# Kernel optimization log

Measured on AMD Instinct MI355X. Metric: run time of the kernel, lower is better.

The kernel has to match this reference:

```python
import jax, jax.numpy as jnp
import numpy as np

BS, L, S, AMB = 64, 64, 63, 32   # batch, sentence len, opseq steps, ambiguities per step
H, E, V, MLP = 128, 300, 50000, 1024
EPS = 1e-8


def setup_inputs() -> dict:
    key = jax.random.key(0)
    ks = jax.random.split(key, 12)
    u = lambda k, shp: jax.random.uniform(k, shp, dtype=jnp.float32) * 0.1
    return {
        "sentences1": jax.random.randint(ks[0], (BS, L), 0, V, dtype=jnp.int32),
        "operations1": jax.random.randint(ks[1], (BS, S, 2 * AMB), 0, L, dtype=jnp.int32),
        "oopl1": jnp.full((BS,), L + S, dtype=jnp.int32),
        "sentences2": jax.random.randint(ks[2], (BS, L), 0, V, dtype=jnp.int32),
        "operations2": jax.random.randint(ks[3], (BS, S, 2 * AMB), 0, L, dtype=jnp.int32),
        "oopl2": jnp.full((BS,), L + S, dtype=jnp.int32),
        "W": u(ks[4], (5 * H, E)),
        "U": u(ks[5], (5 * H, 2 * H)),
        "b": jnp.zeros((5 * H,), dtype=jnp.float32),
        "energy_u": u(ks[6], (H,)),
        "unk_embedding": u(ks[7], (E,)),
        "word_embeddings": jax.random.normal(ks[8], (V, E), dtype=jnp.float32),
        "A": u(ks[9], (MLP, 4 * H)),
        "a": u(ks[10], (MLP,)),
        "inv_temperature": jnp.float32(1.0),
    }


def _gates(preact, ccL, ccR):
    # preact: [..., 5H]; tree-LSTM cell (i, fL, fR, o, u gates)
    i = jax.nn.sigmoid(preact[..., :H])
    fL = jax.nn.sigmoid(preact[..., H:2 * H])
    fR = jax.nn.sigmoid(preact[..., 2 * H:3 * H])
    o = jax.nn.sigmoid(preact[..., 3 * H:4 * H])
    u = jnp.tanh(preact[..., 4 * H:5 * H])
    c = fL * ccL + fR * ccR + i * u
    h = o * jnp.tanh(c)
    return c, h


def _run_chart(sentences, operations, W, U, b, energy_u, unk_embedding,
               word_embeddings, inv_temperature):
    bs = sentences.shape[0]
    # leaf phase: embed each word, preact = W @ emb + b, ccL = ccR = 0
    emb = jnp.where(sentences[..., None] >= 0,
                    word_embeddings[jnp.clip(sentences, 0)], unk_embedding)  # [bs,L,E]
    preact = jnp.einsum('ble,ge->blg', emb, W) + b                            # [bs,L,5H]
    c, h = _gates(preact, 0.0, 0.0)
    chart = jnp.zeros((bs, L + S, 2 * H), dtype=jnp.float32)
    chart = chart.at[:, :L, :].set(jnp.concatenate([c, h], axis=-1))

    def step(chart, inp):
        ops, pos = inp                                   # ops: [bs, 2*AMB], pos: scalar
        entries = jnp.take_along_axis(chart, ops[:, :, None].astype(jnp.int32), axis=1)
        entries = entries.reshape(bs, AMB, 2, 2 * H)     # [bs, amb, (L,R), 2H]
        ccL = entries[:, :, 0, :H]
        ccR = entries[:, :, 1, :H]
        hh = entries[:, :, :, H:].reshape(bs, AMB, 2 * H)  # concat(hL, hR)
        pre = jnp.einsum('bak,gk->bag', hh, U) + b         # [bs, amb, 5H]
        c, h = _gates(pre, ccL, ccR)
        # cosine similarity of h against energy_u
        hn = jnp.maximum(jnp.sqrt(jnp.sum(h * h, axis=-1)), EPS)
        un = jnp.maximum(jnp.sqrt(jnp.sum(energy_u * energy_u)), EPS)
        e = jnp.einsum('bah,h->ba', h, energy_u) / (hn * un)
        s = jax.nn.softmax(e * inv_temperature, axis=1)    # [bs, amb]
        combined = jnp.concatenate([jnp.einsum('ba,bah->bh', s, c),
                                    jnp.einsum('ba,bah->bh', s, h)], axis=-1)
        chart = jax.lax.dynamic_update_slice(chart, combined[:, None, :], (0, pos, 0))
        return chart, None

    ops_seq = jnp.swapaxes(operations, 0, 1)             # [S, bs, 2*AMB]
    positions = L + jnp.arange(S, dtype=jnp.int32)
    chart, _ = jax.lax.scan(step, chart, (ops_seq, positions))
    return chart


def reference(sentences1, operations1, oopl1, sentences2, operations2, oopl2,
              W, U, b, energy_u, unk_embedding, word_embeddings, A, a,
              inv_temperature):
    chart1 = _run_chart(sentences1, operations1, W, U, b, energy_u,
                        unk_embedding, word_embeddings, inv_temperature)
    chart2 = _run_chart(sentences2, operations2, W, U, b, energy_u,
                        unk_embedding, word_embeddings, inv_temperature)
    bs = chart1.shape[0]
    bidx = jnp.arange(bs)
    s1 = chart1[bidx, oopl1 - 1, H:]                     # final composed h, [bs, H]
    s2 = chart2[bidx, oopl2 - 1, H:]
    u = (s1 - s2) ** 2
    v = s1 * s2
    conc = jnp.concatenate([u, v, s1, s2], axis=1)       # [bs, 4H]
    out = jax.nn.relu(jnp.einsum('jk,ik->ij', A, conc) + a)
    return out
```

## Files before the change

kernel.cpp:

```cpp
#include <hip/hip_runtime.h>
#include <hip/hip_bf16.h>

#define BSZ 64
#define LL  64
#define SS  63
#define AMB 32
#define HH  128
#define EE  300
#define MLPN 1024
#define GG  640
#define K2  256
#define PP  127
#define CROW 272

typedef __attribute__((ext_vector_type(8))) short short8;
typedef __attribute__((ext_vector_type(4))) float f32x4;

__device__ __forceinline__ float sigf(float x) { return 1.f / (1.f + __expf(-x)); }

__device__ __forceinline__ unsigned short f2bf(float x) {
    unsigned int u = __float_as_uint(x);
    u += 0x7fffu + ((u >> 16) & 1u);
    return (unsigned short)(u >> 16);
}
__device__ __forceinline__ float bf2f(short x) {
    return __uint_as_float(((unsigned)(unsigned short)x) << 16);
}

#define PW 25600
#define PU 20480
__global__ void __launch_bounds__(256) prep_kernel(
        const float* __restrict__ W, const float* __restrict__ U,
        short* __restrict__ WTB, short* __restrict__ UTB) {
    int idx = blockIdx.x * 256 + threadIdx.x;
    if (idx < PW) {
        int lane = idx & 63, r = idx >> 6;
        int kk = r % 10, n = r / 10;
        int g = n * 16 + (lane & 15);
        int k0 = kk * 32 + ((lane >> 4) << 3);
        const float* src = W + (size_t)g * EE + k0;
        float f[8];
        if (k0 + 8 <= EE) {
            f32x4 x0 = *(const f32x4*)src;
            f32x4 x1 = *(const f32x4*)(src + 4);
            f[0]=x0[0]; f[1]=x0[1]; f[2]=x0[2]; f[3]=x0[3];
            f[4]=x1[0]; f[5]=x1[1]; f[6]=x1[2]; f[7]=x1[3];
        } else {
#pragma unroll
            for (int j = 0; j < 8; ++j) f[j] = (k0 + j < EE) ? src[j] : 0.f;
        }
        short8 v;
#pragma unroll
        for (int j = 0; j < 8; ++j) v[j] = (short)f2bf(f[j]);
        *(short8*)(WTB + (size_t)idx * 8) = v;
    } else if (idx < PW + PU) {
        int o = idx - PW;
        int lane = o & 63, r = o >> 6;
        int kk = r & 7, n = r >> 3;
        int g = n * 16 + (lane & 15);
        int k0 = kk * 32 + ((lane >> 4) << 3);
        const float* src = U + (size_t)g * K2 + k0;
        f32x4 x0 = *(const f32x4*)src;
        f32x4 x1 = *(const f32x4*)(src + 4);
        short8 v;
        v[0]=(short)f2bf(x0[0]); v[1]=(short)f2bf(x0[1]); v[2]=(short)f2bf(x0[2]); v[3]=(short)f2bf(x0[3]);
        v[4]=(short)f2bf(x1[0]); v[5]=(short)f2bf(x1[1]); v[6]=(short)f2bf(x1[2]); v[7]=(short)f2bf(x1[3]);
        *(short8*)(UTB + (size_t)o * 8) = v;
    }
}

__global__ void __launch_bounds__(1024) main_kernel(
        const int* __restrict__ sent1, const int* __restrict__ sent2,
        const int* __restrict__ ops1, const int* __restrict__ ops2,
        const int* __restrict__ oopl1, const int* __restrict__ oopl2,
        const short* __restrict__ WTB, const short* __restrict__ UTB,
        const float* __restrict__ bias, const float* __restrict__ eu,
        const float* __restrict__ invt,
        const float* __restrict__ unk, const float* __restrict__ wemb,
        float* __restrict__ fin) {
    __shared__ __align__(16) short chartL[127 * CROW + 16];
    __shared__ __align__(16) char  buf[40960];
    __shared__ int ops_all[SS * 64];
    __shared__ int sent_lds[64];
    __shared__ unsigned long long smask[64];
    __shared__ int live_list[SS];
    __shared__ float e_num[AMB], h2s[AMB], s_w[AMB];
    __shared__ float comb[2][2][HH];
    __shared__ int nl_sh;
    __shared__ float un_sh;

    short8* AsL = (short8*)buf;
    short8* As2 = (short8*)buf;
    float*  chh = (float*)(buf + 16384);

    const int tid = threadIdx.x;
    const int pair = blockIdx.x, ch = pair >> 6, b = pair & 63;
    const int* sent = ch ? sent2 : sent1;
    const int* ops  = ch ? ops2 : ops1;
    const int* oopl = ch ? oopl2 : oopl1;
    const float it = invt[0];
    const int w = tid >> 6, lane = tid & 63, quad = lane >> 4, l15 = lane & 15;

#pragma unroll
    for (int i = 0; i < 4; ++i) {
        int idx = i * 1024 + tid;
        if (idx < SS * 64) ops_all[idx] = min(max(ops[b * SS * 64 + idx], 0), PP - 1);
    }
    if (tid < 64) sent_lds[tid] = sent[b * LL + tid];
    if (tid < 64) {
        float v = eu[tid] * eu[tid] + eu[tid + 64] * eu[tid + 64];
        for (int off = 32; off >= 1; off >>= 1) v += __shfl_xor(v, off);
        if (tid == 0) un_sh = fmaxf(sqrtf(v), 1e-8f);
    }
    __syncthreads();

#pragma unroll
    for (int i = 0; i < 4; ++i) {
        int t = i * 16 + w;
        if (t < SS) {
            int q = ops_all[t * 64 + lane] - LL;
            unsigned long long bit = (q >= 0 && q < t) ? (1ull << q) : 0ull;
            for (int off = 32; off >= 1; off >>= 1) bit |= __shfl_xor(bit, off);
            if (lane == 0) smask[t] = bit;
        }
    }
    __syncthreads();

    if (tid == 0) {
        unsigned long long mask = 0ull;
        int q0 = oopl[b] - 1 - LL;
        if (q0 >= 0) { if (q0 > SS - 1) q0 = SS - 1; mask = 1ull << q0; }
        for (int t = SS - 1; t >= 1; --t)
            if ((mask >> t) & 1) mask |= smask[t];
        int n = 0;
        for (int t = 0; t < SS; ++t)
            if ((mask >> t) & 1) live_list[n++] = t;
        nl_sh = n;
    }

#pragma unroll
    for (int i = 0; i < 3; ++i) {
        int idx = i * 1024 + tid;
        if (idx < 2142)
            ((int4*)(chartL + 64 * CROW))[idx] = make_int4(0, 0, 0, 0);
    }
    {
        float ef[3][8];
        int est[3], eso[3];
#pragma unroll
        for (int i = 0; i < 3; ++i) {
            int slot = i * 1024 + tid;
            est[i] = -1;
            if (slot < 2560) {
                int t = slot / 40, oct = slot - t * 40;
                est[i] = t; eso[i] = oct;
                int s = sent_lds[t];
                const float* src = (s >= 0) ? (wemb + (size_t)s * EE) : unk;
                int k0 = oct * 8;
                if (k0 + 8 <= EE) {
                    f32x4 x0 = *(const f32x4*)(src + k0);
                    f32x4 x1 = *(const f32x4*)(src + k0 + 4);
                    ef[i][0]=x0[0]; ef[i][1]=x0[1]; ef[i][2]=x0[2]; ef[i][3]=x0[3];
                    ef[i][4]=x1[0]; ef[i][5]=x1[1]; ef[i][6]=x1[2]; ef[i][7]=x1[3];
                } else {
#pragma unroll
                    for (int j = 0; j < 8; ++j) ef[i][j] = (k0 + j < EE) ? src[k0 + j] : 0.f;
                }
            }
        }
#pragma unroll
        for (int i = 0; i < 3; ++i) {
            if (est[i] >= 0) {
                int t = est[i], oct = eso[i];
                short8 v;
#pragma unroll
                for (int j = 0; j < 8; ++j) v[j] = (short)f2bf(ef[i][j]);
                AsL[((t >> 4) * 10 + (oct >> 2)) * 64 + ((oct & 3) << 4) + (t & 15)] = v;
            }
        }
    }
    __syncthreads();

    {
        const int mt = w & 3, nug = w >> 2;
        f32x4 acc[2][3] = {};
        for (int kk = 0; kk < 10; ++kk) {
            short8 a0 = AsL[(mt * 10 + kk) * 64 + lane];
#pragma unroll
            for (int si = 0; si < 3; ++si) {
                int s5 = (si == 0) ? 0 : (si == 1 ? 3 : 4);
#pragma unroll
                for (int hf = 0; hf < 2; ++hf) {
                    int n = (nug + hf * 4) + 8 * s5;
                    short8 bv = *(const short8*)(WTB + ((size_t)(n * 10 + kk) * 64 + lane) * 8);
                    acc[hf][si] = __builtin_amdgcn_mfma_f32_16x16x32_bf16(a0, bv, acc[hf][si], 0, 0, 0);
                }
            }
        }
#pragma unroll
        for (int hf = 0; hf < 2; ++hf) {
            int jc = (nug + hf * 4) * 16 + l15;
            float bi = bias[jc], bo = bias[3 * HH + jc], bu = bias[4 * HH + jc];
#pragma unroll
            for (int r = 0; r < 4; ++r) {
                float pi = acc[hf][0][r] + bi;
                float po = acc[hf][1][r] + bo;
                float pu = acc[hf][2][r] + bu;
                float cv = sigf(pi) * tanhf(pu);
                float hv = sigf(po) * tanhf(cv);
                int l = mt * 16 + quad * 4 + r;
                chartL[l * CROW + jc]      = (short)f2bf(cv);
                chartL[l * CROW + HH + jc] = (short)f2bf(hv);
            }
        }
    }
    __syncthreads();

    const int nl = nl_sh;
    const float eul = eu[lane], euh = eu[64 + lane];
    const int smt = w & 1, snu = w >> 1;
    const int sjc = snu * 16 + l15;
    const float bi  = bias[sjc],          bfl = bias[HH + sjc];
    const float bfr = bias[2 * HH + sjc], bo  = bias[3 * HH + sjc];
    const float bu  = bias[4 * HH + sjc];

    for (int sidx = 0; sidx < nl; ++sidx) {
        const int t = live_list[sidx];
        const int* oprow = ops_all + t * 64;

        {
            int a = tid >> 5, oct = tid & 31, side = oct >> 4, m8 = oct & 15;
            int row = oprow[2 * a + side];
            short8 v = *(const short8*)(chartL + row * CROW + HH + m8 * 8);
            As2[((a >> 4) * 8 + (oct >> 2)) * 64 + ((oct & 3) << 4) + (a & 15)] = v;
        }
        __syncthreads();

        float cvals[4], hvals[4];
        {
            f32x4 acc[5] = {};
            for (int kk = 0; kk < 8; ++kk) {
                short8 a0 = As2[(smt * 8 + kk) * 64 + lane];
#pragma unroll
                for (int s5 = 0; s5 < 5; ++s5) {
                    short8 bv = *(const short8*)(UTB + ((size_t)((snu + 8 * s5) * 8 + kk) * 64 + lane) * 8);
                    acc[s5] = __builtin_amdgcn_mfma_f32_16x16x32_bf16(a0, bv, acc[s5], 0, 0, 0);
                }
            }
#pragma unroll
            for (int r = 0; r < 4; ++r) {
                int a = smt * 16 + quad * 4 + r;
                float ccLv = bf2f(chartL[oprow[2 * a] * CROW + sjc]);
                float ccRv = bf2f(chartL[oprow[2 * a + 1] * CROW + sjc]);
                float cv = sigf(acc[1][r] + bfl) * ccLv
                         + sigf(acc[2][r] + bfr) * ccRv
                         + sigf(acc[0][r] + bi) * tanhf(acc[4][r] + bu);
                float hv = sigf(acc[3][r] + bo) * tanhf(cv);
                cvals[r] = cv; hvals[r] = hv;
                chh[a * 132 + sjc] = hv;
            }
        }
        __syncthreads();

#pragma unroll
        for (int i = 0; i < 2; ++i) {
            int a = w * 2 + i;
            float h0 = chh[a * 132 + lane], h1 = chh[a * 132 + 64 + lane];
            float pe = h0 * eul + h1 * euh;
            float pn = h0 * h0 + h1 * h1;
            for (int off = 32; off >= 1; off >>= 1) {
                pe += __shfl_xor(pe, off);
                pn += __shfl_xor(pn, off);
            }
            if (lane == 0) { e_num[a] = pe; h2s[a] = pn; }
        }
        __syncthreads();

        if (tid < 64) {
            float v = (tid < AMB)
                ? (e_num[tid] / (fmaxf(sqrtf(h2s[tid]), 1e-8f) * un_sh)) * it
                : -3.4e38f;
            float m = v;
            for (int off = 32; off >= 1; off >>= 1) m = fmaxf(m, __shfl_xor(m, off));
            float ex = (tid < AMB) ? __expf(v - m) : 0.f;
            float su = ex;
            for (int off = 32; off >= 1; off >>= 1) su += __shfl_xor(su, off);
            if (tid < AMB) s_w[tid] = ex / su;
        }
        __syncthreads();

        {
            float sc = 0.f, sh = 0.f;
#pragma unroll
            for (int r = 0; r < 4; ++r) {
                int a = smt * 16 + quad * 4 + r;
                float sw = s_w[a];
                sc = fmaf(sw, cvals[r], sc);
                sh = fmaf(sw, hvals[r], sh);
            }
            sc += __shfl_xor(sc, 16); sc += __shfl_xor(sc, 32);
            sh += __shfl_xor(sh, 16); sh += __shfl_xor(sh, 32);
            if (lane < 16) {
                comb[smt][0][sjc] = sc;
                comb[smt][1][sjc] = sh;
            }
        }
        __syncthreads();
        if (tid < K2) {
            int part = tid >> 7, col = tid & 127;
            float val = comb[0][part][col] + comb[1][part][col];
            chartL[(LL + t) * CROW + part * HH + col] = (short)f2bf(val);
        }
        __syncthreads();
    }

    int p = min(max(oopl[b] - 1, 0), PP - 1);
    if (tid < K2)
        fin[(size_t)pair * K2 + tid] = bf2f(chartL[p * CROW + tid]);
}

__global__ void __launch_bounds__(256) mlp_kernel(
        const float* __restrict__ fin,
        const float* __restrict__ A, const float* __restrict__ abias,
        float* __restrict__ out) {
    __shared__ __align__(16) float conc[4][512];
    const int tid = threadIdx.x;
    const int jt = blockIdx.x & 15, bt = blockIdx.x >> 4;

#pragma unroll
    for (int i = 0; i < 2; ++i) {
        int s = i * 256 + tid;
        int bl = s >> 7, kv = s & 127;
        int k0 = kv * 4, sel = k0 >> 7, kk0 = k0 & 127;
        int b = bt * 4 + bl;
        f32x4 s1 = *(const f32x4*)(fin + (size_t)b * K2 + HH + kk0);
        f32x4 s2 = *(const f32x4*)(fin + (size_t)(BSZ + b) * K2 + HH + kk0);
        f32x4 v;
        if (sel == 0)      { f32x4 d = s1 - s2; v = d * d; }
        else if (sel == 1) v = s1 * s2;
        else if (sel == 2) v = s1;
        else               v = s2;
        *(f32x4*)&conc[bl][k0] = v;
    }
    __syncthreads();

    const int jj = tid & 63, bg = tid >> 6;
    const int j = jt * 64 + jj, b = bt * 4 + bg;
    const float* Arow = A + (size_t)j * 512;
    float acc0 = abias[j], acc1 = 0.f;
    for (int k = 0; k < 512; k += 8) {
        f32x4 a0 = *(const f32x4*)(Arow + k);
        f32x4 a1 = *(const f32x4*)(Arow + k + 4);
        f32x4 c0 = *(const f32x4*)&conc[bg][k];
        f32x4 c1 = *(const f32x4*)&conc[bg][k + 4];
#pragma unroll
        for (int u = 0; u < 4; ++u) {
            acc0 = fmaf(a0[u], c0[u], acc0);
            acc1 = fmaf(a1[u], c1[u], acc1);
        }
    }
    out[(size_t)b * MLPN + j] = fmaxf(acc0 + acc1, 0.f);
}

extern "C" void kernel_launch(void* const* d_in, const int* in_sizes, int n_in,
                              void* d_out, int out_size, void* d_ws, size_t ws_size,
                              hipStream_t stream) {
    const int*   sent1 = (const int*)d_in[0];
    const int*   ops1  = (const int*)d_in[1];
    const int*   oopl1 = (const int*)d_in[2];
    const int*   sent2 = (const int*)d_in[3];
    const int*   ops2  = (const int*)d_in[4];
    const int*   oopl2 = (const int*)d_in[5];
    const float* W     = (const float*)d_in[6];
    const float* U     = (const float*)d_in[7];
    const float* bias  = (const float*)d_in[8];
    const float* eu    = (const float*)d_in[9];
    const float* unk   = (const float*)d_in[10];
    const float* wemb  = (const float*)d_in[11];
    const float* A     = (const float*)d_in[12];
    const float* ab    = (const float*)d_in[13];
    const float* invt  = (const float*)d_in[14];
    float* out = (float*)d_out;
    (void)in_sizes; (void)n_in; (void)out_size; (void)ws_size;

    char* ws = (char*)d_ws;
    const size_t WTB_OFF = 0;
    const size_t UTB_OFF = 409600;
    const size_t FIN_OFF = 737280;
    short* WTB = (short*)(ws + WTB_OFF);
    short* UTB = (short*)(ws + UTB_OFF);
    float* fin = (float*)(ws + FIN_OFF);

    prep_kernel<<<180, 256, 0, stream>>>(W, U, WTB, UTB);

    main_kernel<<<128, 1024, 0, stream>>>(sent1, sent2, ops1, ops2, oopl1, oopl2,
                                          WTB, UTB, bias, eu, invt, unk, wemb, fin);

    mlp_kernel<<<256, 256, 0, stream>>>(fin, A, ab, out);
}
```

Before: 186.9 us.

## Split leaf embedding GEMM into separate kernel across 256 blocks

The leaf phase (embedding gather, W projection via MFMA, gate activation) moves out of the per-sentence main kernel into its own kernel. That kernel uses 256 blocks, each handling half of a sentence, and writes bf16 c/h rows to a global chart buffer. The step kernel then loads the chart and ops with vectorized int4 reads. The leaf GEMM loop also double-buffers its W fragment loads. The aim is more parallelism for the leaf phase, since the old kernel used only 128 blocks. The cost is an extra kernel launch and a global round trip for the chart.

```diff
diff --git a/kernel.cpp b/kernel.cpp
--- a/kernel.cpp
+++ b/kernel.cpp
@@ -69,19 +69,104 @@
     }
 }
 
-__global__ void __launch_bounds__(1024) main_kernel(
+__global__ void __launch_bounds__(1024) leaf_kernel(
         const int* __restrict__ sent1, const int* __restrict__ sent2,
+        const short* __restrict__ WTB, const float* __restrict__ bias,
+        const float* __restrict__ unk, const float* __restrict__ wemb,
+        short* __restrict__ chartG) {
+    __shared__ __align__(16) short AsL[2 * 10 * 64 * 8];
+    const int tid = threadIdx.x;
+    const int blk = blockIdx.x, pair = blk >> 1, half = blk & 1;
+    const int ch = pair >> 6, b = pair & 63;
+    const int* sent = ch ? sent2 : sent1;
+    const int w = tid >> 6, lane = tid & 63, quad = lane >> 4, l15 = lane & 15;
+
+    {
+        float ef[2][8];
+        int est[2], eso[2];
+#pragma unroll
+        for (int i = 0; i < 2; ++i) {
+            int slot = i * 1024 + tid;
+            est[i] = -1;
+            if (slot < 1280) {
+                int tloc = slot / 40, oct = slot - tloc * 40;
+                est[i] = tloc; eso[i] = oct;
+                int sid = sent[b * LL + half * 32 + tloc];
+                const float* src = (sid >= 0) ? (wemb + (size_t)sid * EE) : unk;
+                int k0 = oct * 8;
+                if (k0 + 8 <= EE) {
+                    f32x4 x0 = *(const f32x4*)(src + k0);
+                    f32x4 x1 = *(const f32x4*)(src + k0 + 4);
+                    ef[i][0]=x0[0]; ef[i][1]=x0[1]; ef[i][2]=x0[2]; ef[i][3]=x0[3];
+                    ef[i][4]=x1[0]; ef[i][5]=x1[1]; ef[i][6]=x1[2]; ef[i][7]=x1[3];
+                } else {
+#pragma unroll
+                    for (int j = 0; j < 8; ++j) ef[i][j] = (k0 + j < EE) ? src[k0 + j] : 0.f;
+                }
+            }
+        }
+#pragma unroll
+        for (int i = 0; i < 2; ++i) {
+            if (est[i] >= 0) {
+                int tloc = est[i], oct = eso[i];
+                short8 v;
+#pragma unroll
+                for (int j = 0; j < 8; ++j) v[j] = (short)f2bf(ef[i][j]);
+                *(short8*)(AsL + (((tloc >> 4) * 10 + (oct >> 2)) * 64
+                                  + ((oct & 3) << 4) + (tloc & 15)) * 8) = v;
+            }
+        }
+    }
+    __syncthreads();
+
+    const int mt2 = w & 1, nu = w >> 1;
+    f32x4 acc[3] = {};
+    short8 bb0[3], bb1[3];
+#define LDW(dst, kkv) do { \
+    dst[0] = *(const short8*)(WTB + ((size_t)((nu +  0) * 10 + (kkv)) * 64 + lane) * 8); \
+    dst[1] = *(const short8*)(WTB + ((size_t)((nu + 24) * 10 + (kkv)) * 64 + lane) * 8); \
+    dst[2] = *(const short8*)(WTB + ((size_t)((nu + 32) * 10 + (kkv)) * 64 + lane) * 8); \
+} while (0)
+    LDW(bb0, 0);
+#pragma unroll 1
+    for (int kk = 0; kk < 10; kk += 2) {
+        LDW(bb1, kk + 1);
+        short8 a0 = *(const short8*)(AsL + ((mt2 * 10 + kk) * 64 + lane) * 8);
+        acc[0] = __builtin_amdgcn_mfma_f32_16x16x32_bf16(a0, bb0[0], acc[0], 0, 0, 0);
+        acc[1] = __builtin_amdgcn_mfma_f32_16x16x32_bf16(a0, bb0[1], acc[1], 0, 0, 0);
+        acc[2] = __builtin_amdgcn_mfma_f32_16x16x32_bf16(a0, bb0[2], acc[2], 0, 0, 0);
+        if (kk + 2 < 10) LDW(bb0, kk + 2);
+        short8 a1 = *(const short8*)(AsL + ((mt2 * 10 + kk + 1) * 64 + lane) * 8);
+        acc[0] = __builtin_amdgcn_mfma_f32_16x16x32_bf16(a1, bb1[0], acc[0], 0, 0, 0);
+        acc[1] = __builtin_amdgcn_mfma_f32_16x16x32_bf16(a1, bb1[1], acc[1], 0, 0, 0);
+        acc[2] = __builtin_amdgcn_mfma_f32_16x16x32_bf16(a1, bb1[2], acc[2], 0, 0, 0);
+    }
+#undef LDW
+
+    {
+        int jc = nu * 16 + l15;
+        float bi = bias[jc], bo = bias[3 * HH + jc], bu = bias[4 * HH + jc];
+        size_t pb = (size_t)pair * 16384;
+#pragma unroll
+        for (int r = 0; r < 4; ++r) {
+            float cv = sigf(acc[0][r] + bi) * tanhf(acc[2][r] + bu);
+            float hv = sigf(acc[1][r] + bo) * tanhf(cv);
+            int l = half * 32 + mt2 * 16 + quad * 4 + r;
+            chartG[pb + (size_t)l * 256 + jc]      = (short)f2bf(cv);
+            chartG[pb + (size_t)l * 256 + HH + jc] = (short)f2bf(hv);
+        }
+    }
+}
+
+__global__ void __launch_bounds__(1024) step_kernel(
         const int* __restrict__ ops1, const int* __restrict__ ops2,
         const int* __restrict__ oopl1, const int* __restrict__ oopl2,
-        const short* __restrict__ WTB, const short* __restrict__ UTB,
-        const float* __restrict__ bias, const float* __restrict__ eu,
-        const float* __restrict__ invt,
-        const float* __restrict__ unk, const float* __restrict__ wemb,
-        float* __restrict__ fin) {
+        const short* __restrict__ UTB, const float* __restrict__ bias,
+        const float* __restrict__ eu, const float* __restrict__ invt,
+        const short* __restrict__ chartG, float* __restrict__ fin) {
     __shared__ __align__(16) short chartL[127 * CROW + 16];
-    __shared__ __align__(16) char  buf[40960];
-    __shared__ int ops_all[SS * 64];
-    __shared__ int sent_lds[64];
+    __shared__ __align__(16) char  buf[33280];
+    __shared__ __align__(16) int ops_all[SS * 64];
     __shared__ unsigned long long smask[64];
     __shared__ int live_list[SS];
     __shared__ float e_num[AMB], h2s[AMB], s_w[AMB];
@@ -89,28 +174,45 @@
     __shared__ int nl_sh;
     __shared__ float un_sh;
 
-    short8* AsL = (short8*)buf;
     short8* As2 = (short8*)buf;
     float*  chh = (float*)(buf + 16384);
 
     const int tid = threadIdx.x;
     const int pair = blockIdx.x, ch = pair >> 6, b = pair & 63;
-    const int* sent = ch ? sent2 : sent1;
     const int* ops  = ch ? ops2 : ops1;
     const int* oopl = ch ? oopl2 : oopl1;
     const float it = invt[0];
     const int w = tid >> 6, lane = tid & 63, quad = lane >> 4, l15 = lane & 15;
 
-#pragma unroll
-    for (int i = 0; i < 4; ++i) {
-        int idx = i * 1024 + tid;
-        if (idx < SS * 64) ops_all[idx] = min(max(ops[b * SS * 64 + idx], 0), PP - 1);
-    }
-    if (tid < 64) sent_lds[tid] = sent[b * LL + tid];
+    const int4* cg = (const int4*)(chartG + (size_t)pair * 16384);
+    int4 c0 = cg[tid];
+    int4 c1 = cg[1024 + tid];
+    int4 opv = make_int4(0, 0, 0, 0);
+    if (tid < 1008) opv = ((const int4*)(ops + (size_t)b * SS * 64))[tid];
     if (tid < 64) {
         float v = eu[tid] * eu[tid] + eu[tid + 64] * eu[tid + 64];
         for (int off = 32; off >= 1; off >>= 1) v += __shfl_xor(v, off);
         if (tid == 0) un_sh = fmaxf(sqrtf(v), 1e-8f);
+    }
+#pragma unroll
+    for (int i = 0; i < 3; ++i) {
+        int idx = i * 1024 + tid;
+        if (idx < 2142)
+            ((int4*)(chartL + 64 * CROW))[idx] = make_int4(0, 0, 0, 0);
+    }
+    {
+        int r0 = tid >> 5, cq0 = tid & 31;
+        *(int4*)(chartL + r0 * CROW + (cq0 << 3)) = c0;
+        int t2 = 1024 + tid;
+        int r1 = t2 >> 5, cq1 = t2 & 31;
+        *(int4*)(chartL + r1 * CROW + (cq1 << 3)) = c1;
+    }
+    if (tid < 1008) {
+        opv.x = min(max(opv.x, 0), PP - 1);
+        opv.y = min(max(opv.y, 0), PP - 1);
+        opv.z = min(max(opv.z, 0), PP - 1);
+        opv.w = min(max(opv.w, 0), PP - 1);
+        ((int4*)ops_all)[tid] = opv;
     }
     __syncthreads();
 
@@ -136,83 +238,6 @@
         for (int t = 0; t < SS; ++t)
             if ((mask >> t) & 1) live_list[n++] = t;
         nl_sh = n;
-    }
-
-#pragma unroll
-    for (int i = 0; i < 3; ++i) {
-        int idx = i * 1024 + tid;
-        if (idx < 2142)
-            ((int4*)(chartL + 64 * CROW))[idx] = make_int4(0, 0, 0, 0);
-    }
-    {
-        float ef[3][8];
-        int est[3], eso[3];
-#pragma unroll
-        for (int i = 0; i < 3; ++i) {
-            int slot = i * 1024 + tid;
-            est[i] = -1;
-            if (slot < 2560) {
-                int t = slot / 40, oct = slot - t * 40;
-                est[i] = t; eso[i] = oct;
-                int s = sent_lds[t];
-                const float* src = (s >= 0) ? (wemb + (size_t)s * EE) : unk;
-                int k0 = oct * 8;
-                if (k0 + 8 <= EE) {
-                    f32x4 x0 = *(const f32x4*)(src + k0);
-                    f32x4 x1 = *(const f32x4*)(src + k0 + 4);
-                    ef[i][0]=x0[0]; ef[i][1]=x0[1]; ef[i][2]=x0[2]; ef[i][3]=x0[3];
-                    ef[i][4]=x1[0]; ef[i][5]=x1[1]; ef[i][6]=x1[2]; ef[i][7]=x1[3];
-                } else {
-#pragma unroll
-                    for (int j = 0; j < 8; ++j) ef[i][j] = (k0 + j < EE) ? src[k0 + j] : 0.f;
-                }
-            }
-        }
-#pragma unroll
-        for (int i = 0; i < 3; ++i) {
-            if (est[i] >= 0) {
-                int t = est[i], oct = eso[i];
-                short8 v;
-#pragma unroll
-                for (int j = 0; j < 8; ++j) v[j] = (short)f2bf(ef[i][j]);
-                AsL[((t >> 4) * 10 + (oct >> 2)) * 64 + ((oct & 3) << 4) + (t & 15)] = v;
-            }
-        }
-    }
-    __syncthreads();
-
-    {
-        const int mt = w & 3, nug = w >> 2;
-        f32x4 acc[2][3] = {};
-        for (int kk = 0; kk < 10; ++kk) {
-            short8 a0 = AsL[(mt * 10 + kk) * 64 + lane];
-#pragma unroll
-            for (int si = 0; si < 3; ++si) {
-                int s5 = (si == 0) ? 0 : (si == 1 ? 3 : 4);
-#pragma unroll
-                for (int hf = 0; hf < 2; ++hf) {
-                    int n = (nug + hf * 4) + 8 * s5;
-                    short8 bv = *(const short8*)(WTB + ((size_t)(n * 10 + kk) * 64 + lane) * 8);
-                    acc[hf][si] = __builtin_amdgcn_mfma_f32_16x16x32_bf16(a0, bv, acc[hf][si], 0, 0, 0);
-                }
-            }
-        }
-#pragma unroll
-        for (int hf = 0; hf < 2; ++hf) {
-            int jc = (nug + hf * 4) * 16 + l15;
-            float bi = bias[jc], bo = bias[3 * HH + jc], bu = bias[4 * HH + jc];
-#pragma unroll
-            for (int r = 0; r < 4; ++r) {
-                float pi = acc[hf][0][r] + bi;
-                float po = acc[hf][1][r] + bo;
-                float pu = acc[hf][2][r] + bu;
-                float cv = sigf(pi) * tanhf(pu);
-                float hv = sigf(po) * tanhf(cv);
-                int l = mt * 16 + quad * 4 + r;
-                chartL[l * CROW + jc]      = (short)f2bf(cv);
-                chartL[l * CROW + HH + jc] = (short)f2bf(hv);
-            }
-        }
     }
     __syncthreads();
 
@@ -386,15 +411,19 @@
     char* ws = (char*)d_ws;
     const size_t WTB_OFF = 0;
     const size_t UTB_OFF = 409600;
-    const size_t FIN_OFF = 737280;
-    short* WTB = (short*)(ws + WTB_OFF);
-    short* UTB = (short*)(ws + UTB_OFF);
-    float* fin = (float*)(ws + FIN_OFF);
+    const size_t CHG_OFF = 737280;
+    const size_t FIN_OFF = 4931584;
+    short* WTB    = (short*)(ws + WTB_OFF);
+    short* UTB    = (short*)(ws + UTB_OFF);
+    short* chartG = (short*)(ws + CHG_OFF);
+    float* fin    = (float*)(ws + FIN_OFF);
 
     prep_kernel<<<180, 256, 0, stream>>>(W, U, WTB, UTB);
 
-    main_kernel<<<128, 1024, 0, stream>>>(sent1, sent2, ops1, ops2, oopl1, oopl2,
-                                          WTB, UTB, bias, eu, invt, unk, wemb, fin);
+    leaf_kernel<<<256, 1024, 0, stream>>>(sent1, sent2, WTB, bias, unk, wemb, chartG);
+
+    step_kernel<<<128, 1024, 0, stream>>>(ops1, ops2, oopl1, oopl2,
+                                          UTB, bias, eu, invt, chartG, fin);
 
     mlp_kernel<<<256, 256, 0, stream>>>(fin, A, ab, out);
 }
```

Result: no change. 184.3 us (-1.4%).
